# Kernel optimization log

Measured on AMD Instinct MI355X. Metric: run time of the kernel, lower is better.

## Reference

```python
import jax, jax.numpy as jnp
from jax import lax
import numpy as np

B, T, C = 4, 2048, 1024
H = 4                      # num_heads
D = C // H                 # head_dim
EPS_N = 1e-6               # normalizer eps in scan
EPS_GN = 1e-5              # GroupNorm eps (torch default)


def setup_inputs() -> dict:
    key = jax.random.key(0)
    ks = jax.random.split(key, 8)
    s = 0.02
    return {
        "x": jax.random.normal(ks[0], (B, T, C), jnp.float32),
        "conv_w": jax.random.normal(ks[1], (C, 1, 4), jnp.float32) * s,
        "conv_b": jax.random.normal(ks[2], (C,), jnp.float32) * s,
        "wx_w": jax.random.normal(ks[3], (4 * C, C), jnp.float32) * s,
        "wx_b": jax.random.normal(ks[4], (4 * C,), jnp.float32) * s,
        "gn_w": jnp.ones((C,), jnp.float32),
        "gn_b": jnp.zeros((C,), jnp.float32),
        "out_w": jax.random.normal(ks[5], (C, C), jnp.float32) * s,
        "out_b": jax.random.normal(ks[6], (C,), jnp.float32) * s,
    }


def _slstm_scan(i_g, f_g, z_g, o_g):
    # all inputs (B,T,H,D); scan over time
    def step(carry, g):
        c, n, m = carry
        i_t, f_t, z_t, o_t = g
        m_t = jnp.maximum(f_t + m, i_t)
        i_p = jnp.exp(i_t - m_t)
        f_p = jnp.exp(f_t + m - m_t)
        c_t = f_p * c + i_p * z_t
        n_t = f_p * n + i_p
        h_t = jax.nn.sigmoid(o_t) * (c_t / (n_t + EPS_N))
        return (c_t, n_t, m_t), h_t

    tfirst = lambda a: jnp.transpose(a, (1, 0, 2, 3))  # (T,B,H,D)
    init = (jnp.zeros((B, H, D), i_g.dtype),
            jnp.ones((B, H, D), i_g.dtype),
            jnp.zeros((B, H, D), i_g.dtype))
    _, h_seq = lax.scan(step, init, (tfirst(i_g), tfirst(f_g), tfirst(z_g), tfirst(o_g)))
    return jnp.transpose(h_seq, (1, 0, 2, 3))  # (B,T,H,D)


def reference(x, conv_w, conv_b, wx_w, wx_b, gn_w, gn_b, out_w, out_b):
    # causal depthwise conv (torch pad=3 both sides, sliced to first T == left pad 3)
    xc = jnp.transpose(x, (0, 2, 1))  # (B,C,T)
    xc = lax.conv_general_dilated(
        xc, conv_w, window_strides=(1,), padding=[(3, 0)],
        dimension_numbers=("NCH", "OIH", "NCH"), feature_group_count=C)
    xc = jax.nn.silu(xc + conv_b[None, :, None])
    xc = jnp.transpose(xc, (0, 2, 1))  # (B,T,C)

    gates = jnp.einsum("btc,gc->btg", xc, wx_w) + wx_b  # (B,T,4C)
    gates = gates.reshape(B, T, 4, H, D)
    i_g, f_g, z_g, o_g = (gates[:, :, k] for k in range(4))
    z_g = jnp.tanh(z_g)

    h = _slstm_scan(i_g, f_g, z_g, o_g).reshape(B, T, C)

    # GroupNorm(H groups) over (B,C,T): normalize per (batch, group) over (D, T)
    hg = h.reshape(B, T, H, D)
    mean = hg.mean(axis=(1, 3), keepdims=True)
    var = hg.var(axis=(1, 3), keepdims=True)
    hn = ((hg - mean) / jnp.sqrt(var + EPS_GN)).reshape(B, T, C)
    hn = hn * gn_w + gn_b

    out = jnp.einsum("btc,oc->bto", hn, out_w) + out_b
    return out + x  # dropout is identity at inference
```

## Files before the change

kernel.cpp:

```cpp
#include <hip/hip_runtime.h>

#define B_ 4
#define T_ 2048
#define C_ 1024
#define H_ 4
#define D_ 256
#define M_ (B_*T_)
#define N1_ (4*C_)
#define K_ C_
#define LANES_ (B_*C_)
#define CHUNK_ 32
#define NCHUNK_ (T_/CHUNK_)

typedef unsigned short u16;
typedef unsigned int u32;
typedef __bf16 bf16x8 __attribute__((ext_vector_type(8)));
typedef float f32x4 __attribute__((ext_vector_type(4)));
typedef float vf4 __attribute__((ext_vector_type(4)));

__device__ __forceinline__ u16 f2bf(float f) {
  union { float f; u32 u; } v; v.f = f;
  u32 u = v.u;
  u32 r = (u + 0x7FFFu + ((u >> 16) & 1u)) >> 16;
  return (u16)r;
}
__device__ __forceinline__ float b2f(u16 h) {
  union { u32 u; float f; } v; v.u = ((u32)h) << 16;
  return v.f;
}

__global__ void cast_bf16(const float* __restrict__ in, u16* __restrict__ out, int n) {
  int i = blockIdx.x * 256 + threadIdx.x;
  if (i < n) out[i] = f2bf(in[i]);
}

__global__ void conv_silu(const float* __restrict__ x, const float* __restrict__ cw,
                          const float* __restrict__ cb, u16* __restrict__ xc) {
  int idx = blockIdx.x * 256 + threadIdx.x;
  int c = idx & (C_ - 1);
  int t = (idx >> 10) & (T_ - 1);
  float acc = cb[c];
  const float* xp = x + (size_t)idx - 3 * C_;
#pragma unroll
  for (int k = 0; k < 4; ++k) {
    if (t - 3 + k >= 0) acc += cw[c * 4 + k] * xp[(size_t)k * C_];
  }
  float s = acc / (1.f + __expf(-acc));
  xc[idx] = f2bf(s);
}

template <int EPI>
__global__ __launch_bounds__(256, 2)
void gemm_bt(const u16* __restrict__ A, const u16* __restrict__ Bw,
             const float* __restrict__ bias, const float* __restrict__ resid,
             u16* __restrict__ obf, float* __restrict__ of32,
             int M, int N, int K)
{
  __shared__ __align__(16) u16 a_s[128 * 72];
  __shared__ __align__(16) u16 b_s[128 * 72];

  const int tid  = threadIdx.x;
  const int lane = tid & 63;
  const int l15  = lane & 15;
  const int q    = lane >> 4;
  const int wave = tid >> 6;
  const int wm   = (wave >> 1) * 64;
  const int wn   = (wave & 1) * 64;
  const int bm   = blockIdx.y * 128;
  const int bn   = blockIdx.x * 128;

  const int sr = tid >> 3;
  const int sc = (tid & 7) * 8;

  f32x4 acc[4][4];
#pragma unroll
  for (int i = 0; i < 4; ++i)
#pragma unroll
    for (int j = 0; j < 4; ++j) acc[i][j] = (f32x4){0.f, 0.f, 0.f, 0.f};

  for (int k0 = 0; k0 < K; k0 += 64) {
#pragma unroll
    for (int i = 0; i < 4; ++i) {
      int r = sr + i * 32;
      *(vf4*)&a_s[r * 72 + sc] = *(const vf4*)(A + (size_t)(bm + r) * K + k0 + sc);
      *(vf4*)&b_s[r * 72 + sc] = *(const vf4*)(Bw + (size_t)(bn + r) * K + k0 + sc);
    }
    __syncthreads();
#pragma unroll
    for (int kk = 0; kk < 64; kk += 32) {
      bf16x8 af[4], bfr[4];
#pragma unroll
      for (int s = 0; s < 4; ++s)
        af[s] = *(const bf16x8*)&a_s[(wm + s * 16 + l15) * 72 + kk + q * 8];
#pragma unroll
      for (int s = 0; s < 4; ++s)
        bfr[s] = *(const bf16x8*)&b_s[(wn + s * 16 + l15) * 72 + kk + q * 8];
#pragma unroll
      for (int sm = 0; sm < 4; ++sm)
#pragma unroll
        for (int sn = 0; sn < 4; ++sn)
          acc[sm][sn] = __builtin_amdgcn_mfma_f32_16x16x32_bf16(af[sm], bfr[sn], acc[sm][sn], 0, 0, 0);
    }
    __syncthreads();
  }

#pragma unroll
  for (int sm = 0; sm < 4; ++sm) {
#pragma unroll
    for (int r = 0; r < 4; ++r) {
      int row = bm + wm + sm * 16 + q * 4 + r;
#pragma unroll
      for (int sn = 0; sn < 4; ++sn) {
        int col = bn + wn + sn * 16 + l15;
        float v = acc[sm][sn][r] + bias[col];
        if (EPI == 0) {
          if ((col >> 10) == 2) v = tanhf(v);
          obf[(size_t)row * N + col] = f2bf(v);
        } else {
          v += resid[(size_t)row * N + col];
          of32[(size_t)row * N + col] = v;
        }
      }
    }
  }
}

__global__ void scan_passA(const u16* __restrict__ gates,
                           float* __restrict__ sF, float* __restrict__ sM,
                           float* __restrict__ sBc, float* __restrict__ sBn) {
  int tid = blockIdx.x * 256 + threadIdx.x;
  int l = tid & (LANES_ - 1);
  int s = tid >> 12;
  int b = l >> 10, c = l & (C_ - 1);
  const u16* g = gates + (size_t)b * T_ * N1_ + (size_t)(s * CHUNK_) * N1_ + c;
  float F = 0.f, M = -1e30f, bc = 0.f, bn = 0.f;
#pragma unroll 4
  for (int t = 0; t < CHUNK_; ++t) {
    const u16* gt = g + (size_t)t * N1_;
    float i_t = b2f(gt[0]);
    float f_t = b2f(gt[C_]);
    float z_t = b2f(gt[2 * C_]);
    float Mf = M + f_t;
    float Mn = fmaxf(Mf, i_t);
    float ea = __expf(Mf - Mn);
    float eb = __expf(i_t - Mn);
    bc = ea * bc + eb * z_t;
    bn = ea * bn + eb;
    F += f_t;
    M = Mn;
  }
  sF[tid] = F; sM[tid] = M; sBc[tid] = bc; sBn[tid] = bn;
}

__global__ void scan_prefix(const float* __restrict__ sF, const float* __restrict__ sM,
                            const float* __restrict__ sBc, const float* __restrict__ sBn,
                            float* __restrict__ iC, float* __restrict__ iN,
                            float* __restrict__ iM) {
  int l = blockIdx.x * 256 + threadIdx.x;
  float ct = 0.f, nt = 1.f, mt = 0.f;
  for (int s = 0; s < NCHUNK_; ++s) {
    int idx = s * LANES_ + l;
    iC[idx] = ct; iN[idx] = nt; iM[idx] = mt;
    float F = sF[idx], M = sM[idx], bc = sBc[idx], bn = sBn[idx];
    float mf = mt + F;
    float mn = fmaxf(mf, M);
    float a = __expf(mf - mn);
    float bcoef = __expf(M - mn);
    ct = a * ct + bcoef * bc;
    nt = a * nt + bcoef * bn;
    mt = mn;
  }
}

__global__ void scan_passB(const u16* __restrict__ gates,
                           const float* __restrict__ iC, const float* __restrict__ iN,
                           const float* __restrict__ iM, u16* __restrict__ h) {
  int tid = blockIdx.x * 256 + threadIdx.x;
  int l = tid & (LANES_ - 1);
  int s = tid >> 12;
  int b = l >> 10, c = l & (C_ - 1);
  const u16* g = gates + (size_t)b * T_ * N1_ + (size_t)(s * CHUNK_) * N1_ + c;
  u16* hp = h + (size_t)b * T_ * C_ + (size_t)(s * CHUNK_) * C_ + c;
  float cc = iC[tid], nn = iN[tid], mm = iM[tid];
#pragma unroll 4
  for (int t = 0; t < CHUNK_; ++t) {
    const u16* gt = g + (size_t)t * N1_;
    float i_t = b2f(gt[0]);
    float f_t = b2f(gt[C_]);
    float z_t = b2f(gt[2 * C_]);
    float o_t = b2f(gt[3 * C_]);
    float m_new = fmaxf(f_t + mm, i_t);
    float i_p = __expf(i_t - m_new);
    float f_p = __expf(f_t + mm - m_new);
    cc = f_p * cc + i_p * z_t;
    nn = f_p * nn + i_p;
    mm = m_new;
    float sig_o = 1.f / (1.f + __expf(-o_t));
    hp[(size_t)t * C_] = f2bf(sig_o * (cc / (nn + 1e-6f)));
  }
}

__global__ void zero_stats(float* stats) {
  if (threadIdx.x < 32) stats[threadIdx.x] = 0.f;
}

__global__ void stats_kernel(const u16* __restrict__ h, float* __restrict__ stats) {
  int grp = blockIdx.x >> 5;
  int slice = blockIdx.x & 31;
  int b = grp >> 2, hh = grp & 3;
  int d = threadIdx.x;
  const u16* base = h + (size_t)b * T_ * C_ + hh * D_ + d;
  float s = 0.f, sq = 0.f;
  int t0 = slice * 64;
  for (int t = t0; t < t0 + 64; ++t) {
    float v = b2f(base[(size_t)t * C_]);
    s += v; sq += v * v;
  }
  __shared__ float rs[256], rq[256];
  rs[d] = s; rq[d] = sq;
  __syncthreads();
  for (int off = 128; off > 0; off >>= 1) {
    if (d < off) { rs[d] += rs[d + off]; rq[d] += rq[d + off]; }
    __syncthreads();
  }
  if (d == 0) {
    atomicAdd(&stats[grp * 2 + 0], rs[0]);
    atomicAdd(&stats[grp * 2 + 1], rq[0]);
  }
}

__global__ void norm_kernel(const u16* __restrict__ h, const float* __restrict__ stats,
                            const float* __restrict__ gn_w, const float* __restrict__ gn_b,
                            u16* __restrict__ hn) {
  int idx = blockIdx.x * 256 + threadIdx.x;
  int c = idx & (C_ - 1);
  int bt = idx >> 10;
  int b = bt >> 11;
  int hh = c >> 8;
  int grp = b * 4 + hh;
  const float inv_n = 1.f / (float)(T_ * D_);
  float mean = stats[grp * 2 + 0] * inv_n;
  float var  = stats[grp * 2 + 1] * inv_n - mean * mean;
  float rstd = rsqrtf(var + 1e-5f);
  float v = (b2f(h[idx]) - mean) * rstd * gn_w[c] + gn_b[c];
  hn[idx] = f2bf(v);
}

extern "C" void kernel_launch(void* const* d_in, const int* in_sizes, int n_in,
                              void* d_out, int out_size, void* d_ws, size_t ws_size,
                              hipStream_t stream) {
  const float* x      = (const float*)d_in[0];
  const float* conv_w = (const float*)d_in[1];
  const float* conv_b = (const float*)d_in[2];
  const float* wx_w   = (const float*)d_in[3];
  const float* wx_b   = (const float*)d_in[4];
  const float* gn_w   = (const float*)d_in[5];
  const float* gn_b   = (const float*)d_in[6];
  const float* out_w  = (const float*)d_in[7];
  const float* out_b  = (const float*)d_in[8];
  float* out = (float*)d_out;

  char* p = (char*)d_ws;
  u16* xc    = (u16*)p; p += (size_t)M_ * K_ * 2;
  u16* w1    = (u16*)p; p += (size_t)N1_ * K_ * 2;
  u16* w2    = (u16*)p; p += (size_t)C_ * C_ * 2;
  u16* gts   = (u16*)p; p += (size_t)M_ * N1_ * 2;
  u16* hb    = (u16*)p; p += (size_t)M_ * C_ * 2;
  u16* hn    = (u16*)p; p += (size_t)M_ * C_ * 2;
  float* stats = (float*)p; p += 256;
  const int nsum = LANES_ * NCHUNK_;
  float* sF  = (float*)p; p += (size_t)nsum * 4;
  float* sM  = (float*)p; p += (size_t)nsum * 4;
  float* sBc = (float*)p; p += (size_t)nsum * 4;
  float* sBn = (float*)p; p += (size_t)nsum * 4;
  float* iC  = (float*)p; p += (size_t)nsum * 4;
  float* iN  = (float*)p; p += (size_t)nsum * 4;
  float* iM  = (float*)p; p += (size_t)nsum * 4;

  cast_bf16<<<(N1_ * K_) / 256, 256, 0, stream>>>(wx_w, w1, N1_ * K_);
  cast_bf16<<<(C_ * C_) / 256, 256, 0, stream>>>(out_w, w2, C_ * C_);

  conv_silu<<<(M_ * C_) / 256, 256, 0, stream>>>(x, conv_w, conv_b, xc);

  gemm_bt<0><<<dim3(N1_ / 128, M_ / 128), 256, 0, stream>>>(
      xc, w1, wx_b, nullptr, gts, nullptr, M_, N1_, K_);

  scan_passA<<<nsum / 256, 256, 0, stream>>>(gts, sF, sM, sBc, sBn);
  scan_prefix<<<LANES_ / 256, 256, 0, stream>>>(sF, sM, sBc, sBn, iC, iN, iM);
  scan_passB<<<nsum / 256, 256, 0, stream>>>(gts, iC, iN, iM, hb);

  zero_stats<<<1, 64, 0, stream>>>(stats);
  stats_kernel<<<512, 256, 0, stream>>>(hb, stats);
  norm_kernel<<<(M_ * C_) / 256, 256, 0, stream>>>(hb, stats, gn_w, gn_b, hn);

  gemm_bt<1><<<dim3(C_ / 128, M_ / 128), 256, 0, stream>>>(
      hn, w2, out_b, x, nullptr, out, M_, C_, K_);
}
```

Baseline: 329.4 us.

## Vectorize elementwise kernels, fuse GroupNorm stats into scan, use LDS-direct GEMM loads

Vectorizes the weight cast, conv+SiLU and norm kernels so each thread handles 4 or 8 elements. The GEMM now loads tiles with global_load_lds into an XOR-swizzled unpadded LDS layout, and uses an exp-based tanh. The scan passes process two channels per thread with 32-bit loads, and passB accumulates the GroupNorm sums directly, which removes the separate zero_stats and stats_kernel launches and one extra read of h. This cuts launch count and memory traffic, but the direct-to-LDS load path and the swizzle indexing are more complex and carry correctness risk.

```diff
diff --git a/kernel.cpp b/kernel.cpp
--- a/kernel.cpp
+++ b/kernel.cpp
@@ -17,6 +17,8 @@
 typedef __bf16 bf16x8 __attribute__((ext_vector_type(8)));
 typedef float f32x4 __attribute__((ext_vector_type(4)));
 typedef float vf4 __attribute__((ext_vector_type(4)));
+typedef unsigned short u16x4 __attribute__((ext_vector_type(4)));
+typedef unsigned short u16x8 __attribute__((ext_vector_type(8)));
 
 __device__ __forceinline__ u16 f2bf(float f) {
   union { float f; u32 u; } v; v.f = f;
@@ -29,24 +31,45 @@
   return v.f;
 }
 
-__global__ void cast_bf16(const float* __restrict__ in, u16* __restrict__ out, int n) {
-  int i = blockIdx.x * 256 + threadIdx.x;
-  if (i < n) out[i] = f2bf(in[i]);
+__global__ void cast_bf16(const float* __restrict__ in, u16* __restrict__ out) {
+  int i8 = (blockIdx.x * 256 + threadIdx.x) * 8;
+  vf4 a = *(const vf4*)(in + i8);
+  vf4 b = *(const vf4*)(in + i8 + 4);
+  u16x8 o;
+  o[0] = f2bf(a[0]); o[1] = f2bf(a[1]); o[2] = f2bf(a[2]); o[3] = f2bf(a[3]);
+  o[4] = f2bf(b[0]); o[5] = f2bf(b[1]); o[6] = f2bf(b[2]); o[7] = f2bf(b[3]);
+  *(u16x8*)(out + i8) = o;
 }
 
 __global__ void conv_silu(const float* __restrict__ x, const float* __restrict__ cw,
-                          const float* __restrict__ cb, u16* __restrict__ xc) {
-  int idx = blockIdx.x * 256 + threadIdx.x;
-  int c = idx & (C_ - 1);
-  int t = (idx >> 10) & (T_ - 1);
-  float acc = cb[c];
-  const float* xp = x + (size_t)idx - 3 * C_;
+                          const float* __restrict__ cb, u16* __restrict__ xc,
+                          float* __restrict__ stats) {
+  if (blockIdx.x == 0 && threadIdx.x < 32) stats[threadIdx.x] = 0.f;
+  int i4 = (blockIdx.x * 256 + threadIdx.x) * 4;
+  int c = i4 & (C_ - 1);
+  int t = (i4 >> 10) & (T_ - 1);
+  vf4 acc = *(const vf4*)(cb + c);
+  vf4 w0 = *(const vf4*)(cw + (size_t)c * 4);
+  vf4 w1 = *(const vf4*)(cw + (size_t)(c + 1) * 4);
+  vf4 w2 = *(const vf4*)(cw + (size_t)(c + 2) * 4);
+  vf4 w3 = *(const vf4*)(cw + (size_t)(c + 3) * 4);
 #pragma unroll
   for (int k = 0; k < 4; ++k) {
-    if (t - 3 + k >= 0) acc += cw[c * 4 + k] * xp[(size_t)k * C_];
-  }
-  float s = acc / (1.f + __expf(-acc));
-  xc[idx] = f2bf(s);
+    if (t - 3 + k >= 0) {
+      vf4 xv = *(const vf4*)(x + (size_t)i4 + (size_t)(k - 3) * C_);
+      acc[0] = fmaf(w0[k], xv[0], acc[0]);
+      acc[1] = fmaf(w1[k], xv[1], acc[1]);
+      acc[2] = fmaf(w2[k], xv[2], acc[2]);
+      acc[3] = fmaf(w3[k], xv[3], acc[3]);
+    }
+  }
+  u16x4 o;
+#pragma unroll
+  for (int j = 0; j < 4; ++j) {
+    float s = acc[j] / (1.f + __expf(-acc[j]));
+    o[j] = f2bf(s);
+  }
+  *(u16x4*)(xc + i4) = o;
 }
 
 template <int EPI>
@@ -56,8 +79,8 @@
              u16* __restrict__ obf, float* __restrict__ of32,
              int M, int N, int K)
 {
-  __shared__ __align__(16) u16 a_s[128 * 72];
-  __shared__ __align__(16) u16 b_s[128 * 72];
+  __shared__ __align__(16) u16 a_s[128 * 64];
+  __shared__ __align__(16) u16 b_s[128 * 64];
 
   const int tid  = threadIdx.x;
   const int lane = tid & 63;
@@ -69,8 +92,8 @@
   const int bm   = blockIdx.y * 128;
   const int bn   = blockIdx.x * 128;
 
-  const int sr = tid >> 3;
-  const int sc = (tid & 7) * 8;
+  const int srow   = wave * 8 + (lane >> 3);
+  const int schunk = lane & 7;
 
   f32x4 acc[4][4];
 #pragma unroll
@@ -81,20 +104,36 @@
   for (int k0 = 0; k0 < K; k0 += 64) {
 #pragma unroll
     for (int i = 0; i < 4; ++i) {
-      int r = sr + i * 32;
-      *(vf4*)&a_s[r * 72 + sc] = *(const vf4*)(A + (size_t)(bm + r) * K + k0 + sc);
-      *(vf4*)&b_s[r * 72 + sc] = *(const vf4*)(Bw + (size_t)(bn + r) * K + k0 + sc);
+      int r = i * 32 + srow;
+      int lc = schunk ^ (r & 7);
+      const u16* ga = A  + (size_t)(bm + r) * K + k0 + lc * 8;
+      const u16* gb = Bw + (size_t)(bn + r) * K + k0 + lc * 8;
+      __builtin_amdgcn_global_load_lds(
+          (const __attribute__((address_space(1))) u32*)ga,
+          (__attribute__((address_space(3))) u32*)&a_s[(i * 32 + wave * 8) * 64],
+          16, 0, 0);
+      __builtin_amdgcn_global_load_lds(
+          (const __attribute__((address_space(1))) u32*)gb,
+          (__attribute__((address_space(3))) u32*)&b_s[(i * 32 + wave * 8) * 64],
+          16, 0, 0);
     }
     __syncthreads();
 #pragma unroll
     for (int kk = 0; kk < 64; kk += 32) {
+      const int kc = kk >> 3;
       bf16x8 af[4], bfr[4];
 #pragma unroll
-      for (int s = 0; s < 4; ++s)
-        af[s] = *(const bf16x8*)&a_s[(wm + s * 16 + l15) * 72 + kk + q * 8];
-#pragma unroll
-      for (int s = 0; s < 4; ++s)
-        bfr[s] = *(const bf16x8*)&b_s[(wn + s * 16 + l15) * 72 + kk + q * 8];
+      for (int s = 0; s < 4; ++s) {
+        int ra = wm + s * 16 + l15;
+        int ph = (kc + q) ^ (ra & 7);
+        af[s] = *(const bf16x8*)&a_s[ra * 64 + ph * 8];
+      }
+#pragma unroll
+      for (int s = 0; s < 4; ++s) {
+        int rb = wn + s * 16 + l15;
+        int ph = (kc + q) ^ (rb & 7);
+        bfr[s] = *(const bf16x8*)&b_s[rb * 64 + ph * 8];
+      }
 #pragma unroll
       for (int sm = 0; sm < 4; ++sm)
 #pragma unroll
@@ -114,7 +153,10 @@
         int col = bn + wn + sn * 16 + l15;
         float v = acc[sm][sn][r] + bias[col];
         if (EPI == 0) {
-          if ((col >> 10) == 2) v = tanhf(v);
+          if ((col >> 10) == 2) {
+            float e = __expf(2.f * v);
+            v = (e - 1.f) / (e + 1.f);
+          }
           obf[(size_t)row * N + col] = f2bf(v);
         } else {
           v += resid[(size_t)row * N + col];
@@ -129,27 +171,37 @@
                            float* __restrict__ sF, float* __restrict__ sM,
                            float* __restrict__ sBc, float* __restrict__ sBn) {
   int tid = blockIdx.x * 256 + threadIdx.x;
-  int l = tid & (LANES_ - 1);
-  int s = tid >> 12;
-  int b = l >> 10, c = l & (C_ - 1);
-  const u16* g = gates + (size_t)b * T_ * N1_ + (size_t)(s * CHUNK_) * N1_ + c;
-  float F = 0.f, M = -1e30f, bc = 0.f, bn = 0.f;
+  int lp = tid & 2047;
+  int s = tid >> 11;
+  int b = lp >> 9;
+  int c2 = (lp & 511) * 2;
+  const u16* g = gates + (size_t)b * T_ * N1_ + (size_t)(s * CHUNK_) * N1_ + c2;
+  float F0 = 0.f, M0 = -1e30f, bc0 = 0.f, bn0 = 0.f;
+  float F1 = 0.f, M1 = -1e30f, bc1 = 0.f, bn1 = 0.f;
 #pragma unroll 4
   for (int t = 0; t < CHUNK_; ++t) {
     const u16* gt = g + (size_t)t * N1_;
-    float i_t = b2f(gt[0]);
-    float f_t = b2f(gt[C_]);
-    float z_t = b2f(gt[2 * C_]);
-    float Mf = M + f_t;
-    float Mn = fmaxf(Mf, i_t);
-    float ea = __expf(Mf - Mn);
-    float eb = __expf(i_t - Mn);
-    bc = ea * bc + eb * z_t;
-    bn = ea * bn + eb;
-    F += f_t;
-    M = Mn;
-  }
-  sF[tid] = F; sM[tid] = M; sBc[tid] = bc; sBn[tid] = bn;
+    u32 iw = *(const u32*)(gt);
+    u32 fw = *(const u32*)(gt + C_);
+    u32 zw = *(const u32*)(gt + 2 * C_);
+    {
+      float i_t = b2f((u16)iw), f_t = b2f((u16)fw), z_t = b2f((u16)zw);
+      float Mf = M0 + f_t;
+      float Mn = fmaxf(Mf, i_t);
+      float ea = __expf(Mf - Mn), eb = __expf(i_t - Mn);
+      bc0 = ea * bc0 + eb * z_t; bn0 = ea * bn0 + eb; F0 += f_t; M0 = Mn;
+    }
+    {
+      float i_t = b2f((u16)(iw >> 16)), f_t = b2f((u16)(fw >> 16)), z_t = b2f((u16)(zw >> 16));
+      float Mf = M1 + f_t;
+      float Mn = fmaxf(Mf, i_t);
+      float ea = __expf(Mf - Mn), eb = __expf(i_t - Mn);
+      bc1 = ea * bc1 + eb * z_t; bn1 = ea * bn1 + eb; F1 += f_t; M1 = Mn;
+    }
+  }
+  int idx = s * LANES_ + b * C_ + c2;
+  sF[idx] = F0; sM[idx] = M0; sBc[idx] = bc0; sBn[idx] = bn0;
+  sF[idx + 1] = F1; sM[idx + 1] = M1; sBc[idx + 1] = bc1; sBn[idx + 1] = bn1;
 }
 
 __global__ void scan_prefix(const float* __restrict__ sF, const float* __restrict__ sM,
@@ -174,76 +226,91 @@
 
 __global__ void scan_passB(const u16* __restrict__ gates,
                            const float* __restrict__ iC, const float* __restrict__ iN,
-                           const float* __restrict__ iM, u16* __restrict__ h) {
+                           const float* __restrict__ iM, u16* __restrict__ h,
+                           float* __restrict__ stats) {
   int tid = blockIdx.x * 256 + threadIdx.x;
-  int l = tid & (LANES_ - 1);
-  int s = tid >> 12;
-  int b = l >> 10, c = l & (C_ - 1);
-  const u16* g = gates + (size_t)b * T_ * N1_ + (size_t)(s * CHUNK_) * N1_ + c;
-  u16* hp = h + (size_t)b * T_ * C_ + (size_t)(s * CHUNK_) * C_ + c;
-  float cc = iC[tid], nn = iN[tid], mm = iM[tid];
+  int lp = tid & 2047;
+  int s = tid >> 11;
+  int b = lp >> 9;
+  int c2 = (lp & 511) * 2;
+  const u16* g = gates + (size_t)b * T_ * N1_ + (size_t)(s * CHUNK_) * N1_ + c2;
+  u16* hp = h + (size_t)b * T_ * C_ + (size_t)(s * CHUNK_) * C_ + c2;
+  int idx = s * LANES_ + b * C_ + c2;
+  float cc0 = iC[idx], nn0 = iN[idx], mm0 = iM[idx];
+  float cc1 = iC[idx + 1], nn1 = iN[idx + 1], mm1 = iM[idx + 1];
+  float ls = 0.f, lq = 0.f;
 #pragma unroll 4
   for (int t = 0; t < CHUNK_; ++t) {
     const u16* gt = g + (size_t)t * N1_;
-    float i_t = b2f(gt[0]);
-    float f_t = b2f(gt[C_]);
-    float z_t = b2f(gt[2 * C_]);
-    float o_t = b2f(gt[3 * C_]);
-    float m_new = fmaxf(f_t + mm, i_t);
-    float i_p = __expf(i_t - m_new);
-    float f_p = __expf(f_t + mm - m_new);
-    cc = f_p * cc + i_p * z_t;
-    nn = f_p * nn + i_p;
-    mm = m_new;
-    float sig_o = 1.f / (1.f + __expf(-o_t));
-    hp[(size_t)t * C_] = f2bf(sig_o * (cc / (nn + 1e-6f)));
-  }
-}
-
-__global__ void zero_stats(float* stats) {
-  if (threadIdx.x < 32) stats[threadIdx.x] = 0.f;
-}
-
-__global__ void stats_kernel(const u16* __restrict__ h, float* __restrict__ stats) {
-  int grp = blockIdx.x >> 5;
-  int slice = blockIdx.x & 31;
-  int b = grp >> 2, hh = grp & 3;
-  int d = threadIdx.x;
-  const u16* base = h + (size_t)b * T_ * C_ + hh * D_ + d;
-  float s = 0.f, sq = 0.f;
-  int t0 = slice * 64;
-  for (int t = t0; t < t0 + 64; ++t) {
-    float v = b2f(base[(size_t)t * C_]);
-    s += v; sq += v * v;
+    u32 iw = *(const u32*)(gt);
+    u32 fw = *(const u32*)(gt + C_);
+    u32 zw = *(const u32*)(gt + 2 * C_);
+    u32 ow = *(const u32*)(gt + 3 * C_);
+    float h0, h1;
+    {
+      float i_t = b2f((u16)iw), f_t = b2f((u16)fw), z_t = b2f((u16)zw), o_t = b2f((u16)ow);
+      float m_new = fmaxf(f_t + mm0, i_t);
+      float i_p = __expf(i_t - m_new);
+      float f_p = __expf(f_t + mm0 - m_new);
+      cc0 = f_p * cc0 + i_p * z_t;
+      nn0 = f_p * nn0 + i_p;
+      mm0 = m_new;
+      float sig_o = 1.f / (1.f + __expf(-o_t));
+      h0 = sig_o * (cc0 / (nn0 + 1e-6f));
+    }
+    {
+      float i_t = b2f((u16)(iw >> 16)), f_t = b2f((u16)(fw >> 16));
+      float z_t = b2f((u16)(zw >> 16)), o_t = b2f((u16)(ow >> 16));
+      float m_new = fmaxf(f_t + mm1, i_t);
+      float i_p = __expf(i_t - m_new);
+      float f_p = __expf(f_t + mm1 - m_new);
+      cc1 = f_p * cc1 + i_p * z_t;
+      nn1 = f_p * nn1 + i_p;
+      mm1 = m_new;
+      float sig_o = 1.f / (1.f + __expf(-o_t));
+      h1 = sig_o * (cc1 / (nn1 + 1e-6f));
+    }
+    u16 hb0 = f2bf(h0), hb1 = f2bf(h1);
+    float v0 = b2f(hb0), v1 = b2f(hb1);
+    ls += v0 + v1; lq += v0 * v0 + v1 * v1;
+    *(u32*)(hp + (size_t)t * C_) = (u32)hb0 | ((u32)hb1 << 16);
   }
   __shared__ float rs[256], rq[256];
-  rs[d] = s; rq[d] = sq;
+  int thr = threadIdx.x;
+  rs[thr] = ls; rq[thr] = lq;
   __syncthreads();
-  for (int off = 128; off > 0; off >>= 1) {
-    if (d < off) { rs[d] += rs[d + off]; rq[d] += rq[d + off]; }
+  for (int off = 64; off > 0; off >>= 1) {
+    if ((thr & 127) < off) { rs[thr] += rs[thr + off]; rq[thr] += rq[thr + off]; }
     __syncthreads();
   }
-  if (d == 0) {
-    atomicAdd(&stats[grp * 2 + 0], rs[0]);
-    atomicAdd(&stats[grp * 2 + 1], rq[0]);
+  if ((thr & 127) == 0) {
+    int grp = b * 4 + (c2 >> 8);
+    atomicAdd(&stats[grp * 2 + 0], rs[thr]);
+    atomicAdd(&stats[grp * 2 + 1], rq[thr]);
   }
 }
 
 __global__ void norm_kernel(const u16* __restrict__ h, const float* __restrict__ stats,
                             const float* __restrict__ gn_w, const float* __restrict__ gn_b,
                             u16* __restrict__ hn) {
-  int idx = blockIdx.x * 256 + threadIdx.x;
-  int c = idx & (C_ - 1);
-  int bt = idx >> 10;
-  int b = bt >> 11;
-  int hh = c >> 8;
-  int grp = b * 4 + hh;
+  int i8 = (blockIdx.x * 256 + threadIdx.x) * 8;
+  int c = i8 & (C_ - 1);
+  int b = i8 >> 21;
+  int grp = b * 4 + (c >> 8);
   const float inv_n = 1.f / (float)(T_ * D_);
   float mean = stats[grp * 2 + 0] * inv_n;
   float var  = stats[grp * 2 + 1] * inv_n - mean * mean;
   float rstd = rsqrtf(var + 1e-5f);
-  float v = (b2f(h[idx]) - mean) * rstd * gn_w[c] + gn_b[c];
-  hn[idx] = f2bf(v);
+  u16x8 hv = *(const u16x8*)(h + i8);
+  vf4 w0 = *(const vf4*)(gn_w + c), w1 = *(const vf4*)(gn_w + c + 4);
+  vf4 b0 = *(const vf4*)(gn_b + c), b1 = *(const vf4*)(gn_b + c + 4);
+  u16x8 o;
+#pragma unroll
+  for (int j = 0; j < 4; ++j) {
+    o[j]     = f2bf((b2f(hv[j])     - mean) * rstd * w0[j] + b0[j]);
+    o[j + 4] = f2bf((b2f(hv[j + 4]) - mean) * rstd * w1[j] + b1[j]);
+  }
+  *(u16x8*)(hn + i8) = o;
 }
 
 extern "C" void kernel_launch(void* const* d_in, const int* in_sizes, int n_in,
@@ -277,21 +344,19 @@
   float* iN  = (float*)p; p += (size_t)nsum * 4;
   float* iM  = (float*)p; p += (size_t)nsum * 4;
 
-  cast_bf16<<<(N1_ * K_) / 256, 256, 0, stream>>>(wx_w, w1, N1_ * K_);
-  cast_bf16<<<(C_ * C_) / 256, 256, 0, stream>>>(out_w, w2, C_ * C_);
-
-  conv_silu<<<(M_ * C_) / 256, 256, 0, stream>>>(x, conv_w, conv_b, xc);
+  cast_bf16<<<(N1_ * K_) / 2048, 256, 0, stream>>>(wx_w, w1);
+  cast_bf16<<<(C_ * C_) / 2048, 256, 0, stream>>>(out_w, w2);
+
+  conv_silu<<<(M_ * C_) / 1024, 256, 0, stream>>>(x, conv_w, conv_b, xc, stats);
 
   gemm_bt<0><<<dim3(N1_ / 128, M_ / 128), 256, 0, stream>>>(
       xc, w1, wx_b, nullptr, gts, nullptr, M_, N1_, K_);
 
-  scan_passA<<<nsum / 256, 256, 0, stream>>>(gts, sF, sM, sBc, sBn);
+  scan_passA<<<(2048 * NCHUNK_) / 256, 256, 0, stream>>>(gts, sF, sM, sBc, sBn);
   scan_prefix<<<LANES_ / 256, 256, 0, stream>>>(sF, sM, sBc, sBn, iC, iN, iM);
-  scan_passB<<<nsum / 256, 256, 0, stream>>>(gts, iC, iN, iM, hb);
-
-  zero_stats<<<1, 64, 0, stream>>>(stats);
-  stats_kernel<<<512, 256, 0, stream>>>(hb, stats);
-  norm_kernel<<<(M_ * C_) / 256, 256, 0, stream>>>(hb, stats, gn_w, gn_b, hn);
+  scan_passB<<<(2048 * NCHUNK_) / 256, 256, 0, stream>>>(gts, iC, iN, iM, hb, stats);
+
+  norm_kernel<<<(M_ * C_) / 2048, 256, 0, stream>>>(hb, stats, gn_w, gn_b, hn);
 
   gemm_bt<1><<<dim3(C_ / 128, M_ / 128), 256, 0, stream>>>(
       hn, w2, out_b, x, nullptr, out, M_, C_, K_);
```

Result: faster. 287.5 us (-12.7%).
